# Kernel tuning notes

Measured on AMD Instinct MI355X. Metric: run time of the kernel, lower is better.

## Reference

```python
import jax, jax.numpy as jnp
import numpy as np

B, T, D, V, MEM = 2, 512, 512, 256, 256


def _gru(x, h0, wih, whh, bih, bhh):
    # x: [B,T,D], h0: [B,D]; torch GRU gate order: r, z, n
    def step(h, xt):
        gi = xt @ wih.T + bih            # [B,3D]
        gh = h @ whh.T + bhh             # [B,3D]
        i_r, i_z, i_n = jnp.split(gi, 3, axis=-1)
        h_r, h_z, h_n = jnp.split(gh, 3, axis=-1)
        r = jax.nn.sigmoid(i_r + h_r)
        z = jax.nn.sigmoid(i_z + h_z)
        n = jnp.tanh(i_n + r * h_n)
        h_new = (1.0 - z) * n + z * h
        return h_new, h_new
    hT, ys = jax.lax.scan(step, h0, jnp.swapaxes(x, 0, 1))
    return jnp.swapaxes(ys, 0, 1), hT


def _layernorm(x, g, b, eps=1e-5):
    m = jnp.mean(x, axis=-1, keepdims=True)
    v = jnp.mean((x - m) ** 2, axis=-1, keepdims=True)
    return (x - m) / jnp.sqrt(v + eps) * g + b


def setup_inputs() -> dict:
    key = jax.random.key(0)
    ks = jax.random.split(key, 24)
    s = 1.0 / np.sqrt(D)
    inp = {
        'x': jax.random.randint(ks[0], (B, T), 0, V, dtype=jnp.int32),
        'h_f': jnp.zeros((1, B, D), jnp.float32),
        'h_s': jnp.zeros((1, B, D), jnp.float32),
        'soma_w': jax.random.normal(ks[1], (V, D), jnp.float32),
        'fast_wih': jax.random.normal(ks[2], (3 * D, D)) * s,
        'fast_whh': jax.random.normal(ks[3], (3 * D, D)) * s,
        'fast_bih': jax.random.normal(ks[4], (3 * D,)) * s,
        'fast_bhh': jax.random.normal(ks[5], (3 * D,)) * s,
        'slow_wih': jax.random.normal(ks[6], (3 * D, D)) * s,
        'slow_whh': jax.random.normal(ks[7], (3 * D, D)) * s,
        'slow_bih': jax.random.normal(ks[8], (3 * D,)) * s,
        'slow_bhh': jax.random.normal(ks[9], (3 * D,)) * s,
        'qkv_w': jax.random.normal(ks[10], (3 * D, D)) * s,
        'qkv_b': jax.random.normal(ks[11], (3 * D,)) * s,
        'gate_w': jax.random.normal(ks[12], (D, D)) * s,
        'gate_b': jax.random.normal(ks[13], (D,)) * s,
        'gate_g': jnp.ones((D,), jnp.float32),
        'gate_bb': jnp.zeros((D,), jnp.float32),
        'mem_bank': jax.random.normal(ks[14], (MEM, D)) * 0.1,
        'hip_qw': jax.random.normal(ks[15], (D, D)) * s,
        'hip_qb': jax.random.normal(ks[16], (D,)) * s,
        'axon_w': jax.random.normal(ks[17], (D, 4 * D)) * (0.5 * s),
        'axon_b': jax.random.normal(ks[18], (D,)) * s,
        'norm_g': jnp.ones((D,), jnp.float32),
        'norm_b': jnp.zeros((D,), jnp.float32),
    }
    return inp


def reference(x, h_f, h_s, soma_w, fast_wih, fast_whh, fast_bih, fast_bhh,
              slow_wih, slow_whh, slow_bih, slow_bhh, qkv_w, qkv_b,
              gate_w, gate_b, gate_g, gate_bb, mem_bank, hip_qw, hip_qb,
              axon_w, axon_b, norm_g, norm_b):
    d = soma_w.shape[1]
    s_in = soma_w[x]  # mod[0] == 1.0
    p_f, hf1 = _gru(s_in, h_f[0], fast_wih, fast_whh, fast_bih, fast_bhh)
    p_s, hs1 = _gru(p_f, h_s[0], slow_wih, slow_whh, slow_bih, slow_bhh)
    # LinearIntentMemory: naive cumulative outer-product linear attention
    qkv = p_s @ qkv_w.T + qkv_b
    q, k, v = jnp.split(qkv, 3, axis=-1)
    q = jax.nn.elu(q) + 1.0
    k = jax.nn.elu(k) + 1.0
    kv_cum = jnp.cumsum(jnp.einsum('bti,btj->btij', k, v), axis=1)  # [B,T,D,D]
    num = jnp.einsum('bti,btij->btj', q, kv_cum)
    den = jnp.einsum('bti,bti->bt', q, jnp.cumsum(k, axis=1))[..., None] + 1e-6
    l_mem = num / den
    # intent gate: Linear -> LayerNorm -> Tanh
    intent = jnp.tanh(_layernorm(p_s @ gate_w.T + gate_b, gate_g, gate_bb))
    # hippocampus: softmax attention over memory bank
    qh = p_s @ hip_qw.T + hip_qb
    attn = qh @ mem_bank.T / jnp.sqrt(jnp.float32(d))
    episodes = jax.nn.softmax(attn, axis=-1) @ mem_bank
    combined = jnp.concatenate([p_f, intent, l_mem, episodes], axis=-1)
    thought = _layernorm(jnp.tanh(combined @ axon_w.T + axon_b), norm_g, norm_b)
    sw = soma_w / jnp.maximum(jnp.linalg.norm(soma_w, axis=-1, keepdims=True), 1e-12)
    logits = (thought @ sw.T) * 16.0
    return (logits, thought, hf1[None], hs1[None])
```

## Files before the change

kernel.cpp:

```cpp
#include <hip/hip_runtime.h>
#include <cstddef>

#define F_ELUQK 1
#define F_CAUSAL 2
#define F_DIV 4
#define F_NN 8
#define F_SCALE 16
#define F_ROWSUM 32
#define FLAG_STRIDE 32
#define L_WGS 64
#define UNITS 8

enum : int {
  OFF_QH = 0,
  OFF_COMB = 524288,
  OFF_PS = OFF_COMB + 2097152,
  OFF_QKV = OFF_PS + 524288,
  OFF_SCORES = OFF_QKV + 1572864,
  OFF_DEN = OFF_SCORES + 524288,
  OFF_TMP = OFF_DEN + 1024,
  OFF_ATTN = OFF_TMP + 524288,
  OFF_SWN = OFF_ATTN + 262144,
  OFF_RING = OFF_SWN + 256,
  OFF_HSB = OFF_RING + 8192,
  OFF_FLAGS = OFF_HSB + 4096
};

__global__ __launch_bounds__(256) void gemm(
    const float* __restrict__ A, int lda, const float* __restrict__ B, int ldb,
    float* __restrict__ C, int ldc, int coff, int K,
    const float* __restrict__ bias, const float* __restrict__ den,
    const float* __restrict__ cscale, float* __restrict__ rsum,
    float scale, int flags, int bBatch,
    float* __restrict__ Cz, int kzoff) {
  __shared__ float As[16 * 65];
  __shared__ float Bs[16 * 65];
  int tid = threadIdx.x;
  int n0 = blockIdx.x * 64, m0 = blockIdx.y * 64;
  if (blockIdx.z) { A += kzoff; B += kzoff; C = Cz; bias = nullptr; }
  int rowoff = (m0 >> 9) * bBatch;
  int tx = tid & 15, ty = tid >> 4;

  if ((flags & F_CAUSAL) && n0 > ((m0 & 511) + 63)) {
    #pragma unroll
    for (int i = 0; i < 4; ++i)
      #pragma unroll
      for (int j = 0; j < 4; ++j)
        C[(size_t)(m0 + ty * 4 + i) * ldc + coff + n0 + tx * 4 + j] = 0.f;
    return;
  }

  float acc[4][4] = {};
  for (int k0 = 0; k0 < K; k0 += 16) {
    {
      int rr = tid >> 2, c4 = (tid & 3) << 2;
      const float* ap = A + (size_t)(m0 + rr) * lda + (k0 + c4);
      float4 av = *(const float4*)ap;
      As[(c4 + 0) * 65 + rr] = av.x;
      As[(c4 + 1) * 65 + rr] = av.y;
      As[(c4 + 2) * 65 + rr] = av.z;
      As[(c4 + 3) * 65 + rr] = av.w;
    }
    if (!(flags & F_NN)) {
      int rr = tid >> 2, c4 = (tid & 3) << 2;
      const float* bp = B + (size_t)(n0 + rr + rowoff) * ldb + (k0 + c4);
      float4 bv = *(const float4*)bp;
      Bs[(c4 + 0) * 65 + rr] = bv.x; Bs[(c4 + 1) * 65 + rr] = bv.y;
      Bs[(c4 + 2) * 65 + rr] = bv.z; Bs[(c4 + 3) * 65 + rr] = bv.w;
    } else {
      int kk = tid >> 4, n4 = (tid & 15) << 2;
      const float* bp = B + (size_t)(k0 + kk + rowoff) * ldb + (n0 + n4);
      float4 bv = *(const float4*)bp;
      Bs[kk * 65 + n4 + 0] = bv.x; Bs[kk * 65 + n4 + 1] = bv.y;
      Bs[kk * 65 + n4 + 2] = bv.z; Bs[kk * 65 + n4 + 3] = bv.w;
    }
    __syncthreads();
    #pragma unroll
    for (int k = 0; k < 16; ++k) {
      float av[4], bv[4];
      #pragma unroll
      for (int i = 0; i < 4; ++i) av[i] = As[k * 65 + ty * 4 + i];
      #pragma unroll
      for (int j = 0; j < 4; ++j) bv[j] = Bs[k * 65 + tx * 4 + j];
      #pragma unroll
      for (int i = 0; i < 4; ++i)
        #pragma unroll
        for (int j = 0; j < 4; ++j)
          acc[i][j] = fmaf(av[i], bv[j], acc[i][j]);
    }
    __syncthreads();
  }
  float rs[4] = {0.f, 0.f, 0.f, 0.f};
  #pragma unroll
  for (int i = 0; i < 4; ++i) {
    int m = m0 + ty * 4 + i;
    float dv = (flags & F_DIV) ? (1.0f / (den[m] + 1e-6f)) : 1.0f;
    #pragma unroll
    for (int j = 0; j < 4; ++j) {
      int n = n0 + tx * 4 + j;
      float v = acc[i][j];
      if (bias) v += bias[n];
      if (flags & F_ELUQK) { if (n < 1024) v = (v > 0.f) ? (v + 1.f) : __expf(v); }
      if (flags & F_CAUSAL) { if (n > (m & 511)) v = 0.f; }
      if (flags & F_SCALE) v *= scale;
      if (cscale) v *= cscale[coff + n];
      if (flags & F_DIV) v *= dv;
      C[(size_t)m * ldc + coff + n] = v;
      if (flags & F_ROWSUM) rs[i] += v;
    }
  }
  if (flags & F_ROWSUM) {
    #pragma unroll
    for (int i = 0; i < 4; ++i) {
      float s = rs[i];
      s += __shfl_xor(s, 1); s += __shfl_xor(s, 2);
      s += __shfl_xor(s, 4); s += __shfl_xor(s, 8);
      if (tx == 0) atomicAdd(rsum + (m0 + ty * 4 + i), s);
    }
  }
}

__global__ __launch_bounds__(256) void gemm3(
    const float* __restrict__ A,
    const float* __restrict__ qkvw, const float* __restrict__ qkvb,
    const float* __restrict__ gatew, const float* __restrict__ gateb,
    const float* __restrict__ hipw, const float* __restrict__ hipb,
    float* __restrict__ QKV, float* __restrict__ TMP, float* __restrict__ QH) {
  __shared__ float As[16 * 65];
  __shared__ float Bs[16 * 65];
  int tid = threadIdx.x;
  int n0 = blockIdx.x * 64, m0 = blockIdx.y * 64;
  const float* B; const float* bias; float* C; int ldc, base;
  if (n0 < 1536) { B = qkvw; bias = qkvb; C = QKV; ldc = 1536; base = 0; }
  else if (n0 < 2048) { B = gatew; bias = gateb; C = TMP; ldc = 512; base = 1536; }
  else { B = hipw; bias = hipb; C = QH; ldc = 512; base = 2048; }
  int tx = tid & 15, ty = tid >> 4;
  float acc[4][4] = {};
  for (int k0 = 0; k0 < 512; k0 += 16) {
    {
      int rr = tid >> 2, c4 = (tid & 3) << 2;
      const float* ap = A + (size_t)(m0 + rr) * 512 + (k0 + c4);
      float4 av = *(const float4*)ap;
      As[(c4 + 0) * 65 + rr] = av.x; As[(c4 + 1) * 65 + rr] = av.y;
      As[(c4 + 2) * 65 + rr] = av.z; As[(c4 + 3) * 65 + rr] = av.w;
    }
    {
      int rr = tid >> 2, c4 = (tid & 3) << 2;
      const float* bp = B + (size_t)(n0 - base + rr) * 512 + (k0 + c4);
      float4 bv = *(const float4*)bp;
      Bs[(c4 + 0) * 65 + rr] = bv.x; Bs[(c4 + 1) * 65 + rr] = bv.y;
      Bs[(c4 + 2) * 65 + rr] = bv.z; Bs[(c4 + 3) * 65 + rr] = bv.w;
    }
    __syncthreads();
    #pragma unroll
    for (int k = 0; k < 16; ++k) {
      float av[4], bv[4];
      #pragma unroll
      for (int i = 0; i < 4; ++i) av[i] = As[k * 65 + ty * 4 + i];
      #pragma unroll
      for (int j = 0; j < 4; ++j) bv[j] = Bs[k * 65 + tx * 4 + j];
      #pragma unroll
      for (int i = 0; i < 4; ++i)
        #pragma unroll
        for (int j = 0; j < 4; ++j)
          acc[i][j] = fmaf(av[i], bv[j], acc[i][j]);
    }
    __syncthreads();
  }
  #pragma unroll
  for (int i = 0; i < 4; ++i) {
    int m = m0 + ty * 4 + i;
    #pragma unroll
    for (int j = 0; j < 4; ++j) {
      int n = n0 + tx * 4 + j;
      float v = acc[i][j] + bias[n - base];
      if (n < 1024) v = (v > 0.f) ? (v + 1.f) : __expf(v);
      C[(size_t)m * ldc + (n - base)] = v;
    }
  }
}

__device__ __forceinline__ void post_flag(unsigned* flags, int w, unsigned v) {
  __hip_atomic_store(flags + (size_t)w * FLAG_STRIDE, v, __ATOMIC_RELAXED,
                     __HIP_MEMORY_SCOPE_AGENT);
}
__device__ __forceinline__ void poll64(const unsigned* flags, unsigned tgt, int lane) {
  const unsigned* p = flags + (size_t)lane * FLAG_STRIDE;
  while (__hip_atomic_load(p, __ATOMIC_RELAXED, __HIP_MEMORY_SCOPE_AGENT) < tgt)
    __builtin_amdgcn_s_sleep(1);
}

__global__ __launch_bounds__(256, 1) void gru2_kernel(
    const float* __restrict__ soma, const int* __restrict__ x,
    const float* __restrict__ fwih, const float* __restrict__ fbih,
    const float* __restrict__ fwhh, const float* __restrict__ fbhh,
    const float* __restrict__ h0f,
    const float* __restrict__ swih, const float* __restrict__ sbih,
    const float* __restrict__ swhh, const float* __restrict__ sbhh,
    const float* __restrict__ h0s,
    float* __restrict__ pf_out,
    float* __restrict__ ps_out,
    float* __restrict__ hfT, float* __restrict__ hsT,
    unsigned long long* __restrict__ ringq,
    unsigned long long* __restrict__ hsq,
    unsigned* __restrict__ flagsB) {
  __shared__ __attribute__((aligned(16))) float hl[1024];
  __shared__ __attribute__((aligned(16))) float inb[2048];
  __shared__ float P[48];
  __shared__ float Q[48];
  __shared__ float bl[24];
  __shared__ float bi[24];
  __shared__ int xl[1024];
  int tid = threadIdx.x, wg = blockIdx.x;
  bool L1 = wg < L_WGS;
  int j0 = (wg & (L_WGS - 1)) * UNITS;
  int part = tid & 7, r = tid >> 3;
  int g = r >> 3, u = r & 7;
  int wave = tid >> 6, lane = tid & 63;
  const float* whh = L1 ? fwhh : swhh;
  const float* bhh = L1 ? fbhh : sbhh;
  const float* wih = L1 ? fwih : swih;
  const float* bih = L1 ? fbih : sbih;

  float4 wh[16], wi[16];
  if (r < 24) {
    const float* wp = whh + (size_t)(g * 512 + j0 + u) * 512 + part * 4;
    #pragma unroll
    for (int i = 0; i < 16; ++i) wh[i] = *(const float4*)(wp + i * 32);
    const float* wp2 = wih + (size_t)(g * 512 + j0 + u) * 512 + part * 4;
    #pragma unroll
    for (int i = 0; i < 16; ++i) wi[i] = *(const float4*)(wp2 + i * 32);
  }
  if (tid < 24) {
    bl[tid] = bhh[(tid >> 3) * 512 + j0 + (tid & 7)];
    bi[tid] = bih[(tid >> 3) * 512 + j0 + (tid & 7)];
  }
  if (L1) {
    for (int q = tid; q < 1024; q += 256) xl[q] = x[q];
  }
  __syncthreads();

  const float4* h4 = (const float4*)hl;

  if (L1) {
    for (int t = 0; t < 512; ++t) {
      if (wave == 0) {
        if (t == 0) {
          #pragma unroll
          for (int k = 0; k < 16; ++k) hl[k * 64 + lane] = h0f[k * 64 + lane];
        } else {
          const unsigned long long* s8 = ringq + (size_t)((t - 1) & 3) * 1024;
          unsigned expect = (unsigned)t;
          unsigned long long v[16];
          for (;;) {
            #pragma unroll
            for (int k = 0; k < 16; ++k)
              v[k] = __hip_atomic_load(s8 + k * 64 + lane, __ATOMIC_RELAXED,
                                       __HIP_MEMORY_SCOPE_AGENT);
            unsigned bad = 0;
            #pragma unroll
            for (int k = 0; k < 16; ++k) bad |= ((unsigned)(v[k] >> 32)) ^ expect;
            if (__all(bad == 0)) break;
            __builtin_amdgcn_s_sleep(1);
          }
          #pragma unroll
          for (int k = 0; k < 16; ++k)
            hl[k * 64 + lane] = __uint_as_float((unsigned)v[k]);
        }
      } else if (wave == 1) {
        if (t >= 4) poll64(flagsB, (unsigned)(t - 3), lane);
      } else {
        int b = wave - 2;
        if (t == 0) {
          int row0 = xl[b * 512];
          const float4* sp = (const float4*)(soma + (size_t)row0 * 512);
          float4* dst = (float4*)(inb + b * 512);
          dst[lane * 2] = sp[lane * 2]; dst[lane * 2 + 1] = sp[lane * 2 + 1];
        }
        if (t + 1 < 512) {
          int row = xl[b * 512 + t + 1];
          const float4* sp = (const float4*)(soma + (size_t)row * 512);
          float4* dst = (float4*)(inb + ((t + 1) & 1) * 1024 + b * 512);
          dst[lane * 2] = sp[lane * 2]; dst[lane * 2 + 1] = sp[lane * 2 + 1];
        }
      }
      __syncthreads();
      if (r < 24) {
        const float4* f4v = (const float4*)(inb + (t & 1) * 1024);
        float a0 = 0.f, a1 = 0.f, c0 = 0.f, c1 = 0.f;
        #pragma unroll
        for (int i = 0; i < 16; ++i) {
          float4 w = wh[i];
          float4 x0 = h4[i * 8 + part];
          float4 x1 = h4[128 + i * 8 + part];
          a0 += w.x * x0.x + w.y * x0.y + w.z * x0.z + w.w * x0.w;
          a1 += w.x * x1.x + w.y * x1.y + w.z * x1.z + w.w * x1.w;
          float4 v = wi[i];
          float4 y0 = f4v[i * 8 + part];
          float4 y1 = f4v[128 + i * 8 + part];
          c0 += v.x * y0.x + v.y * y0.y + v.z * y0.z + v.w * y0.w;
          c1 += v.x * y1.x + v.y * y1.y + v.z * y1.z + v.w * y1.w;
        }
        a0 += __shfl_xor(a0, 1); a0 += __shfl_xor(a0, 2); a0 += __shfl_xor(a0, 4);
        a1 += __shfl_xor(a1, 1); a1 += __shfl_xor(a1, 2); a1 += __shfl_xor(a1, 4);
        c0 += __shfl_xor(c0, 1); c0 += __shfl_xor(c0, 2); c0 += __shfl_xor(c0, 4);
        c1 += __shfl_xor(c1, 1); c1 += __shfl_xor(c1, 2); c1 += __shfl_xor(c1, 4);
        if (part == 0) { P[r] = a0; P[24 + r] = a1; Q[r] = c0; Q[24 + r] = c1; }
      }
      __syncthreads();
      if (tid < 16) {
        int b = tid >> 3, u2 = tid & 7, j = j0 + u2;
        float i_r = Q[b * 24 + u2] + bi[u2];
        float i_z = Q[b * 24 + 8 + u2] + bi[8 + u2];
        float i_n = Q[b * 24 + 16 + u2] + bi[16 + u2];
        float gh_r = P[b * 24 + u2] + bl[u2];
        float gh_z = P[b * 24 + 8 + u2] + bl[8 + u2];
        float gh_n = P[b * 24 + 16 + u2] + bl[16 + u2];
        float hold = hl[b * 512 + j];
        float rg = 1.0f / (1.0f + __expf(-(i_r + gh_r)));
        float zg = 1.0f / (1.0f + __expf(-(i_z + gh_z)));
        float ng = tanhf(i_n + rg * gh_n);
        float hnew = (1.0f - zg) * ng + zg * hold;
        unsigned long long pv =
            ((unsigned long long)(unsigned)(t + 1) << 32) |
            (unsigned long long)__float_as_uint(hnew);
        __hip_atomic_store(ringq + (size_t)(t & 3) * 1024 + b * 512 + j, pv,
                           __ATOMIC_RELAXED, __HIP_MEMORY_SCOPE_AGENT);
        pf_out[(size_t)(b * 512 + t) * 2048 + j] = hnew;
        if (t == 511) hfT[b * 512 + j] = hnew;
      }
      __asm__ __volatile__("s_barrier" ::: "memory");
    }
  } else {
    for (int t2 = 0; t2 < 512; ++t2) {
      if (wave == 0) {
        const unsigned long long* f8 = ringq + (size_t)(t2 & 3) * 1024;
        unsigned expect = (unsigned)(t2 + 1);
        unsigned long long v[16];
        for (;;) {
          #pragma unroll
          for (int k = 0; k < 16; ++k)
            v[k] = __hip_atomic_load(f8 + k * 64 + lane, __ATOMIC_RELAXED,
                                     __HIP_MEMORY_SCOPE_AGENT);
          unsigned bad = 0;
          #pragma unroll
          for (int k = 0; k < 16; ++k) bad |= ((unsigned)(v[k] >> 32)) ^ expect;
          if (__all(bad == 0)) break;
          __builtin_amdgcn_s_sleep(1);
        }
        #pragma unroll
        for (int k = 0; k < 16; ++k)
          inb[(t2 & 1) * 1024 + k * 64 + lane] = __uint_as_float((unsigned)v[k]);
        if (lane == 0) post_flag(flagsB, wg - L_WGS, (unsigned)(t2 + 1));
      } else if (wave == 1) {
        if (t2 == 0) {
          #pragma unroll
          for (int k = 0; k < 16; ++k) hl[k * 64 + lane] = h0s[k * 64 + lane];
        } else {
          const unsigned long long* s8 = hsq + (size_t)((t2 - 1) & 1) * 1024;
          unsigned expect = (unsigned)t2;
          unsigned long long v[16];
          for (;;) {
            #pragma unroll
            for (int k = 0; k < 16; ++k)
              v[k] = __hip_atomic_load(s8 + k * 64 + lane, __ATOMIC_RELAXED,
                                       __HIP_MEMORY_SCOPE_AGENT);
            unsigned bad = 0;
            #pragma unroll
            for (int k = 0; k < 16; ++k) bad |= ((unsigned)(v[k] >> 32)) ^ expect;
            if (__all(bad == 0)) break;
            __builtin_amdgcn_s_sleep(1);
          }
          #pragma unroll
          for (int k = 0; k < 16; ++k)
            hl[k * 64 + lane] = __uint_as_float((unsigned)v[k]);
        }
      }
      __syncthreads();
      if (r < 24) {
        const float4* f4v = (const float4*)(inb + (t2 & 1) * 1024);
        float a0 = 0.f, a1 = 0.f, c0 = 0.f, c1 = 0.f;
        #pragma unroll
        for (int i = 0; i < 16; ++i) {
          float4 w = wh[i];
          float4 x0 = h4[i * 8 + part];
          float4 x1 = h4[128 + i * 8 + part];
          a0 += w.x * x0.x + w.y * x0.y + w.z * x0.z + w.w * x0.w;
          a1 += w.x * x1.x + w.y * x1.y + w.z * x1.z + w.w * x1.w;
          float4 v = wi[i];
          float4 y0 = f4v[i * 8 + part];
          float4 y1 = f4v[128 + i * 8 + part];
          c0 += v.x * y0.x + v.y * y0.y + v.z * y0.z + v.w * y0.w;
          c1 += v.x * y1.x + v.y * y1.y + v.z * y1.z + v.w * y1.w;
        }
        a0 += __shfl_xor(a0, 1); a0 += __shfl_xor(a0, 2); a0 += __shfl_xor(a0, 4);
        a1 += __shfl_xor(a1, 1); a1 += __shfl_xor(a1, 2); a1 += __shfl_xor(a1, 4);
        c0 += __shfl_xor(c0, 1); c0 += __shfl_xor(c0, 2); c0 += __shfl_xor(c0, 4);
        c1 += __shfl_xor(c1, 1); c1 += __shfl_xor(c1, 2); c1 += __shfl_xor(c1, 4);
        if (part == 0) { P[r] = a0; P[24 + r] = a1; Q[r] = c0; Q[24 + r] = c1; }
      }
      __syncthreads();
      if (tid < 16) {
        int b = tid >> 3, u2 = tid & 7, j = j0 + u2;
        float i_r = Q[b * 24 + u2] + bi[u2];
        float i_z = Q[b * 24 + 8 + u2] + bi[8 + u2];
        float i_n = Q[b * 24 + 16 + u2] + bi[16 + u2];
        float gh_r = P[b * 24 + u2] + bl[u2];
        float gh_z = P[b * 24 + 8 + u2] + bl[8 + u2];
        float gh_n = P[b * 24 + 16 + u2] + bl[16 + u2];
        float hold = hl[b * 512 + j];
        float rg = 1.0f / (1.0f + __expf(-(i_r + gh_r)));
        float zg = 1.0f / (1.0f + __expf(-(i_z + gh_z)));
        float ng = tanhf(i_n + rg * gh_n);
        float hnew = (1.0f - zg) * ng + zg * hold;
        unsigned long long pv =
            ((unsigned long long)(unsigned)(t2 + 1) << 32) |
            (unsigned long long)__float_as_uint(hnew);
        __hip_atomic_store(hsq + (size_t)(t2 & 1) * 1024 + b * 512 + j, pv,
                           __ATOMIC_RELAXED, __HIP_MEMORY_SCOPE_AGENT);
        ps_out[(size_t)(b * 512 + t2) * 512 + j] = hnew;
        if (t2 == 511) hsT[b * 512 + j] = hnew;
      }
      __asm__ __volatile__("s_barrier" ::: "memory");
    }
  }
}

__global__ __launch_bounds__(256) void softmax_kernel(float* __restrict__ a) {
  int m = blockIdx.x, tid = threadIdx.x;
  float v = a[(size_t)m * 256 + tid];
  float mx = v;
  #pragma unroll
  for (int off = 32; off > 0; off >>= 1) mx = fmaxf(mx, __shfl_down(mx, off));
  __shared__ float r4[4];
  __shared__ float s4[4];
  if ((tid & 63) == 0) r4[tid >> 6] = mx;
  __syncthreads();
  mx = fmaxf(fmaxf(r4[0], r4[1]), fmaxf(r4[2], r4[3]));
  float e = __expf(v - mx);
  float s = e;
  #pragma unroll
  for (int off = 32; off > 0; off >>= 1) s += __shfl_down(s, off);
  if ((tid & 63) == 0) s4[tid >> 6] = s;
  __syncthreads();
  s = s4[0] + s4[1] + s4[2] + s4[3];
  a[(size_t)m * 256 + tid] = e / s;
}

__global__ __launch_bounds__(256) void ln_kernel(
    const float* __restrict__ src, const float* __restrict__ src2,
    float* __restrict__ dst, int ldd, int dcoff,
    const float* __restrict__ gv, const float* __restrict__ bv, int tanhFirst) {
  int m = blockIdx.x, tid = threadIdx.x;
  float x0 = src[(size_t)m * 512 + tid];
  float x1 = src[(size_t)m * 512 + 256 + tid];
  if (src2) { x0 += src2[(size_t)m * 512 + tid]; x1 += src2[(size_t)m * 512 + 256 + tid]; }
  if (tanhFirst) { x0 = tanhf(x0); x1 = tanhf(x1); }
  float s = x0 + x1, ss = x0 * x0 + x1 * x1;
  #pragma unroll
  for (int off = 32; off > 0; off >>= 1) { s += __shfl_down(s, off); ss += __shfl_down(ss, off); }
  __shared__ float rs[4], rss[4];
  if ((tid & 63) == 0) { rs[tid >> 6] = s; rss[tid >> 6] = ss; }
  __syncthreads();
  float st = rs[0] + rs[1] + rs[2] + rs[3];
  float sst = rss[0] + rss[1] + rss[2] + rss[3];
  float mean = st * (1.0f / 512.0f);
  float var = sst * (1.0f / 512.0f) - mean * mean;
  float inv = rsqrtf(var + 1e-5f);
  float y0 = (x0 - mean) * inv * gv[tid] + bv[tid];
  float y1 = (x1 - mean) * inv * gv[256 + tid] + bv[256 + tid];
  if (!tanhFirst) { y0 = tanhf(y0); y1 = tanhf(y1); }
  dst[(size_t)m * ldd + dcoff + tid] = y0;
  dst[(size_t)m * ldd + dcoff + 256 + tid] = y1;
}

__global__ __launch_bounds__(256) void swinv_kernel(const float* __restrict__ soma,
                                                    float* __restrict__ swn) {
  int r = blockIdx.x, tid = threadIdx.x;
  float x0 = soma[(size_t)r * 512 + tid];
  float x1 = soma[(size_t)r * 512 + 256 + tid];
  float ss = x0 * x0 + x1 * x1;
  #pragma unroll
  for (int off = 32; off > 0; off >>= 1) ss += __shfl_down(ss, off);
  __shared__ float r4[4];
  if ((tid & 63) == 0) r4[tid >> 6] = ss;
  __syncthreads();
  if (tid == 0) {
    float norm = fmaxf(sqrtf(r4[0] + r4[1] + r4[2] + r4[3]), 1e-12f);
    swn[r] = 16.0f / norm;
  }
}

extern "C" void kernel_launch(void* const* d_in, const int* in_sizes, int n_in,
                              void* d_out, int out_size, void* d_ws, size_t ws_size,
                              hipStream_t stream) {
  (void)in_sizes; (void)n_in; (void)out_size; (void)ws_size;
  float* W = (float*)d_ws;
  float* outf = (float*)d_out;
  const int* x = (const int*)d_in[0];
  const float* soma = (const float*)d_in[3];

  hipMemsetAsync((char*)d_ws + (size_t)OFF_RING * 4, 0, 57344, stream);
  hipMemsetAsync((char*)d_ws + (size_t)OFF_DEN * 4, 0, 4096, stream);

  gru2_kernel<<<2 * L_WGS, 256, 0, stream>>>(soma, x,
      (const float*)d_in[4], (const float*)d_in[6],
      (const float*)d_in[5], (const float*)d_in[7], (const float*)d_in[1],
      (const float*)d_in[8], (const float*)d_in[10],
      (const float*)d_in[9], (const float*)d_in[11], (const float*)d_in[2],
      W + OFF_COMB, W + OFF_PS, outf + 786432, outf + 787456,
      (unsigned long long*)(W + OFF_RING), (unsigned long long*)(W + OFF_HSB),
      (unsigned*)(W + OFF_FLAGS));

  gemm3<<<dim3(40, 16), 256, 0, stream>>>(W + OFF_PS,
      (const float*)d_in[12], (const float*)d_in[13],
      (const float*)d_in[14], (const float*)d_in[15],
      (const float*)d_in[19], (const float*)d_in[20],
      W + OFF_QKV, W + OFF_TMP, W + OFF_QH);

  gemm<<<dim3(8, 16), 256, 0, stream>>>(W + OFF_QKV, 1536, W + OFF_QKV + 512, 1536,
      W + OFF_SCORES, 512, 0, 512, nullptr, nullptr, nullptr, W + OFF_DEN,
      1.f, F_CAUSAL | F_ROWSUM, 512, nullptr, 0);

  gemm<<<dim3(8, 16), 256, 0, stream>>>(W + OFF_SCORES, 512, W + OFF_QKV + 1024, 1536,
      W + OFF_COMB, 2048, 1024, 512, nullptr, W + OFF_DEN, nullptr, nullptr,
      1.f, F_NN | F_DIV, 512, nullptr, 0);

  ln_kernel<<<1024, 256, 0, stream>>>(W + OFF_TMP, nullptr, W + OFF_COMB, 2048, 512,
      (const float*)d_in[16], (const float*)d_in[17], 0);

  gemm<<<dim3(4, 16), 256, 0, stream>>>(W + OFF_QH, 512, (const float*)d_in[18], 512,
      W + OFF_ATTN, 256, 0, 512, nullptr, nullptr, nullptr, nullptr,
      0.04419417382415922f, F_SCALE, 0, nullptr, 0);
  softmax_kernel<<<1024, 256, 0, stream>>>(W + OFF_ATTN);
  gemm<<<dim3(8, 16), 256, 0, stream>>>(W + OFF_ATTN, 256, (const float*)d_in[18], 512,
      W + OFF_COMB, 2048, 1536, 256, nullptr, nullptr, nullptr, nullptr,
      1.f, F_NN, 0, nullptr, 0);

  gemm<<<dim3(8, 16, 2), 256, 0, stream>>>(W + OFF_COMB, 2048, (const float*)d_in[21], 2048,
      W + OFF_TMP, 512, 0, 1024, (const float*)d_in[22], nullptr, nullptr, nullptr,
      1.f, 0, 0, W + OFF_QH, 1024);

  ln_kernel<<<1024, 256, 0, stream>>>(W + OFF_TMP, W + OFF_QH, outf + 262144, 512, 0,
      (const float*)d_in[23], (const float*)d_in[24], 1);

  swinv_kernel<<<256, 256, 0, stream>>>(soma, W + OFF_SWN);
  gemm<<<dim3(4, 16), 256, 0, stream>>>(outf + 262144, 512, soma, 512,
      outf, 256, 0, 512, nullptr, nullptr, W + OFF_SWN, nullptr,
      1.f, 0, 0, nullptr, 0);
}
```

Before: 2.104 ms.

## Restructure GRU step pipeline: precompute input projection before barrier, add per-WG flags

Reorganizes the persistent two-layer GRU kernel so waves 0-2 compute the input-side projection (wih·x) before the first barrier while wave 3 polls for the previous hidden state. The input fetch for the next step, including the slow layer's read of the fast ring, moves into the slot after the barrier, overlapping with the recurrent matvec. Per-workgroup flags (flagsA) are added so the ring is polled on cheap flag words before the tagged 64-bit loads. Barriers become lgkmcnt-wait plus s_barrier. This aims to take the input projection and prefetch off the serial critical path, at the cost of an extra flag store per step and a larger zeroed region.

Result: faster. 1.790 ms (-14.9%).

```diff
diff --git a/kernel.cpp b/kernel.cpp
--- a/kernel.cpp
+++ b/kernel.cpp
@@ -25,6 +25,8 @@
   OFF_HSB = OFF_RING + 8192,
   OFF_FLAGS = OFF_HSB + 4096
 };
+
+#define BAR() __asm__ __volatile__("s_waitcnt lgkmcnt(0)\n\ts_barrier" ::: "memory")
 
 __global__ __launch_bounds__(256) void gemm(
     const float* __restrict__ A, int lda, const float* __restrict__ B, int ldb,
@@ -189,6 +191,25 @@
   while (__hip_atomic_load(p, __ATOMIC_RELAXED, __HIP_MEMORY_SCOPE_AGENT) < tgt)
     __builtin_amdgcn_s_sleep(1);
 }
+__device__ __forceinline__ void tagload16(const unsigned long long* __restrict__ src,
+                                          unsigned expect, int lane,
+                                          float* __restrict__ dstLds) {
+  unsigned long long v[16];
+  for (;;) {
+    #pragma unroll
+    for (int k = 0; k < 16; ++k)
+      v[k] = __hip_atomic_load(src + k * 64 + lane, __ATOMIC_RELAXED,
+                               __HIP_MEMORY_SCOPE_AGENT);
+    unsigned bad = 0;
+    #pragma unroll
+    for (int k = 0; k < 16; ++k) bad |= ((unsigned)(v[k] >> 32)) ^ expect;
+    if (__all(bad == 0)) break;
+    __builtin_amdgcn_s_sleep(1);
+  }
+  #pragma unroll
+  for (int k = 0; k < 16; ++k)
+    dstLds[k * 64 + lane] = __uint_as_float((unsigned)v[k]);
+}
 
 __global__ __launch_bounds__(256, 1) void gru2_kernel(
     const float* __restrict__ soma, const int* __restrict__ x,
@@ -203,7 +224,7 @@
     float* __restrict__ hfT, float* __restrict__ hsT,
     unsigned long long* __restrict__ ringq,
     unsigned long long* __restrict__ hsq,
-    unsigned* __restrict__ flagsB) {
+    unsigned* __restrict__ flagsA, unsigned* __restrict__ flagsB) {
   __shared__ __attribute__((aligned(16))) float hl[1024];
   __shared__ __attribute__((aligned(16))) float inb[2048];
   __shared__ float P[48];
@@ -240,54 +261,48 @@
   }
   __syncthreads();
 
+  if (wave == 3) {
+    if (L1) {
+      int r0 = xl[0], r1 = xl[512];
+      const float4* sp0 = (const float4*)(soma + (size_t)r0 * 512);
+      const float4* sp1 = (const float4*)(soma + (size_t)r1 * 512);
+      float4* dst = (float4*)inb;
+      dst[lane * 2] = sp0[lane * 2]; dst[lane * 2 + 1] = sp0[lane * 2 + 1];
+      dst[128 + lane * 2] = sp1[lane * 2]; dst[128 + lane * 2 + 1] = sp1[lane * 2 + 1];
+    } else {
+      poll64(flagsA, 1u, lane);
+      tagload16(ringq, 1u, lane, inb);
+    }
+  }
+  BAR();
+
   const float4* h4 = (const float4*)hl;
 
   if (L1) {
     for (int t = 0; t < 512; ++t) {
-      if (wave == 0) {
+      float c0 = 0.f, c1 = 0.f;
+      if (wave == 3) {
         if (t == 0) {
           #pragma unroll
           for (int k = 0; k < 16; ++k) hl[k * 64 + lane] = h0f[k * 64 + lane];
         } else {
-          const unsigned long long* s8 = ringq + (size_t)((t - 1) & 3) * 1024;
-          unsigned expect = (unsigned)t;
-          unsigned long long v[16];
-          for (;;) {
-            #pragma unroll
-            for (int k = 0; k < 16; ++k)
-              v[k] = __hip_atomic_load(s8 + k * 64 + lane, __ATOMIC_RELAXED,
-                                       __HIP_MEMORY_SCOPE_AGENT);
-            unsigned bad = 0;
-            #pragma unroll
-            for (int k = 0; k < 16; ++k) bad |= ((unsigned)(v[k] >> 32)) ^ expect;
-            if (__all(bad == 0)) break;
-            __builtin_amdgcn_s_sleep(1);
-          }
-          #pragma unroll
-          for (int k = 0; k < 16; ++k)
-            hl[k * 64 + lane] = __uint_as_float((unsigned)v[k]);
-        }
-      } else if (wave == 1) {
-        if (t >= 4) poll64(flagsB, (unsigned)(t - 3), lane);
+          poll64(flagsA, (unsigned)t, lane);
+          tagload16(ringq + (size_t)((t - 1) & 3) * 1024, (unsigned)t, lane, hl);
+        }
       } else {
-        int b = wave - 2;
-        if (t == 0) {
-          int row0 = xl[b * 512];
-          const float4* sp = (const float4*)(soma + (size_t)row0 * 512);
-          float4* dst = (float4*)(inb + b * 512);
-          dst[lane * 2] = sp[lane * 2]; dst[lane * 2 + 1] = sp[lane * 2 + 1];
-        }
-        if (t + 1 < 512) {
-          int row = xl[b * 512 + t + 1];
-          const float4* sp = (const float4*)(soma + (size_t)row * 512);
-          float4* dst = (float4*)(inb + ((t + 1) & 1) * 1024 + b * 512);
-          dst[lane * 2] = sp[lane * 2]; dst[lane * 2 + 1] = sp[lane * 2 + 1];
+        const float4* f4v = (const float4*)(inb + (t & 1) * 1024);
+        #pragma unroll
+        for (int i = 0; i < 16; ++i) {
+          float4 v = wi[i];
+          float4 y0 = f4v[i * 8 + part];
+          float4 y1 = f4v[128 + i * 8 + part];
+          c0 += v.x * y0.x + v.y * y0.y + v.z * y0.z + v.w * y0.w;
+          c1 += v.x * y1.x + v.y * y1.y + v.z * y1.z + v.w * y1.w;
         }
       }
-      __syncthreads();
-      if (r < 24) {
-        const float4* f4v = (const float4*)(inb + (t & 1) * 1024);
-        float a0 = 0.f, a1 = 0.f, c0 = 0.f, c1 = 0.f;
+      BAR();
+      if (wave != 3) {
+        float a0 = 0.f, a1 = 0.f;
         #pragma unroll
         for (int i = 0; i < 16; ++i) {
           float4 w = wh[i];
@@ -295,21 +310,30 @@
           float4 x1 = h4[128 + i * 8 + part];
           a0 += w.x * x0.x + w.y * x0.y + w.z * x0.z + w.w * x0.w;
           a1 += w.x * x1.x + w.y * x1.y + w.z * x1.z + w.w * x1.w;
-          float4 v = wi[i];
-          float4 y0 = f4v[i * 8 + part];
-          float4 y1 = f4v[128 + i * 8 + part];
-          c0 += v.x * y0.x + v.y * y0.y + v.z * y0.z + v.w * y0.w;
-          c1 += v.x * y1.x + v.y * y1.y + v.z * y1.z + v.w * y1.w;
         }
         a0 += __shfl_xor(a0, 1); a0 += __shfl_xor(a0, 2); a0 += __shfl_xor(a0, 4);
         a1 += __shfl_xor(a1, 1); a1 += __shfl_xor(a1, 2); a1 += __shfl_xor(a1, 4);
         c0 += __shfl_xor(c0, 1); c0 += __shfl_xor(c0, 2); c0 += __shfl_xor(c0, 4);
         c1 += __shfl_xor(c1, 1); c1 += __shfl_xor(c1, 2); c1 += __shfl_xor(c1, 4);
         if (part == 0) { P[r] = a0; P[24 + r] = a1; Q[r] = c0; Q[24 + r] = c1; }
+      } else {
+        if (t + 1 < 512) {
+          int r0 = xl[t + 1], r1 = xl[512 + t + 1];
+          const float4* sp0 = (const float4*)(soma + (size_t)r0 * 512);
+          const float4* sp1 = (const float4*)(soma + (size_t)r1 * 512);
+          float4 p0 = sp0[lane * 2], p1 = sp0[lane * 2 + 1];
+          float4 p2 = sp1[lane * 2], p3 = sp1[lane * 2 + 1];
+          if (t >= 4) poll64(flagsB, (unsigned)(t - 3), lane);
+          float4* dst = (float4*)(inb + ((t + 1) & 1) * 1024);
+          dst[lane * 2] = p0; dst[lane * 2 + 1] = p1;
+          dst[128 + lane * 2] = p2; dst[128 + lane * 2 + 1] = p3;
+        } else {
+          if (t >= 4) poll64(flagsB, (unsigned)(t - 3), lane);
+        }
       }
-      __syncthreads();
-      if (tid < 16) {
-        int b = tid >> 3, u2 = tid & 7, j = j0 + u2;
+      BAR();
+      if (wave == 3 && lane < 16) {
+        int b = lane >> 3, u2 = lane & 7, j = j0 + u2;
         float i_r = Q[b * 24 + u2] + bi[u2];
         float i_z = Q[b * 24 + 8 + u2] + bi[8 + u2];
         float i_n = Q[b * 24 + 16 + u2] + bi[16 + u2];
@@ -326,60 +350,36 @@
             (unsigned long long)__float_as_uint(hnew);
         __hip_atomic_store(ringq + (size_t)(t & 3) * 1024 + b * 512 + j, pv,
                            __ATOMIC_RELAXED, __HIP_MEMORY_SCOPE_AGENT);
+        if (lane == 0) post_flag(flagsA, wg, (unsigned)(t + 1));
         pf_out[(size_t)(b * 512 + t) * 2048 + j] = hnew;
         if (t == 511) hfT[b * 512 + j] = hnew;
       }
-      __asm__ __volatile__("s_barrier" ::: "memory");
     }
   } else {
     for (int t2 = 0; t2 < 512; ++t2) {
-      if (wave == 0) {
-        const unsigned long long* f8 = ringq + (size_t)(t2 & 3) * 1024;
-        unsigned expect = (unsigned)(t2 + 1);
-        unsigned long long v[16];
-        for (;;) {
-          #pragma unroll
-          for (int k = 0; k < 16; ++k)
-            v[k] = __hip_atomic_load(f8 + k * 64 + lane, __ATOMIC_RELAXED,
-                                     __HIP_MEMORY_SCOPE_AGENT);
-          unsigned bad = 0;
-          #pragma unroll
-          for (int k = 0; k < 16; ++k) bad |= ((unsigned)(v[k] >> 32)) ^ expect;
-          if (__all(bad == 0)) break;
-          __builtin_amdgcn_s_sleep(1);
-        }
-        #pragma unroll
-        for (int k = 0; k < 16; ++k)
-          inb[(t2 & 1) * 1024 + k * 64 + lane] = __uint_as_float((unsigned)v[k]);
-        if (lane == 0) post_flag(flagsB, wg - L_WGS, (unsigned)(t2 + 1));
-      } else if (wave == 1) {
+      float c0 = 0.f, c1 = 0.f;
+      if (wave == 3) {
         if (t2 == 0) {
           #pragma unroll
           for (int k = 0; k < 16; ++k) hl[k * 64 + lane] = h0s[k * 64 + lane];
         } else {
-          const unsigned long long* s8 = hsq + (size_t)((t2 - 1) & 1) * 1024;
-          unsigned expect = (unsigned)t2;
-          unsigned long long v[16];
-          for (;;) {
-            #pragma unroll
-            for (int k = 0; k < 16; ++k)
-              v[k] = __hip_atomic_load(s8 + k * 64 + lane, __ATOMIC_RELAXED,
-                                       __HIP_MEMORY_SCOPE_AGENT);
-            unsigned bad = 0;
-            #pragma unroll
-            for (int k = 0; k < 16; ++k) bad |= ((unsigned)(v[k] >> 32)) ^ expect;
-            if (__all(bad == 0)) break;
-            __builtin_amdgcn_s_sleep(1);
-          }
-          #pragma unroll
-          for (int k = 0; k < 16; ++k)
-            hl[k * 64 + lane] = __uint_as_float((unsigned)v[k]);
+          poll64(flagsB, (unsigned)t2, lane);
+          tagload16(hsq + (size_t)((t2 - 1) & 1) * 1024, (unsigned)t2, lane, hl);
+        }
+      } else {
+        const float4* f4v = (const float4*)(inb + (t2 & 1) * 1024);
+        #pragma unroll
+        for (int i = 0; i < 16; ++i) {
+          float4 v = wi[i];
+          float4 y0 = f4v[i * 8 + part];
+          float4 y1 = f4v[128 + i * 8 + part];
+          c0 += v.x * y0.x + v.y * y0.y + v.z * y0.z + v.w * y0.w;
+          c1 += v.x * y1.x + v.y * y1.y + v.z * y1.z + v.w * y1.w;
         }
       }
-      __syncthreads();
-      if (r < 24) {
-        const float4* f4v = (const float4*)(inb + (t2 & 1) * 1024);
-        float a0 = 0.f, a1 = 0.f, c0 = 0.f, c1 = 0.f;
+      BAR();
+      if (wave != 3) {
+        float a0 = 0.f, a1 = 0.f;
         #pragma unroll
         for (int i = 0; i < 16; ++i) {
           float4 w = wh[i];
@@ -387,21 +387,22 @@
           float4 x1 = h4[128 + i * 8 + part];
           a0 += w.x * x0.x + w.y * x0.y + w.z * x0.z + w.w * x0.w;
           a1 += w.x * x1.x + w.y * x1.y + w.z * x1.z + w.w * x1.w;
-          float4 v = wi[i];
-          float4 y0 = f4v[i * 8 + part];
-          float4 y1 = f4v[128 + i * 8 + part];
-          c0 += v.x * y0.x + v.y * y0.y + v.z * y0.z + v.w * y0.w;
-          c1 += v.x * y1.x + v.y * y1.y + v.z * y1.z + v.w * y1.w;
         }
         a0 += __shfl_xor(a0, 1); a0 += __shfl_xor(a0, 2); a0 += __shfl_xor(a0, 4);
         a1 += __shfl_xor(a1, 1); a1 += __shfl_xor(a1, 2); a1 += __shfl_xor(a1, 4);
         c0 += __shfl_xor(c0, 1); c0 += __shfl_xor(c0, 2); c0 += __shfl_xor(c0, 4);
         c1 += __shfl_xor(c1, 1); c1 += __shfl_xor(c1, 2); c1 += __shfl_xor(c1, 4);
         if (part == 0) { P[r] = a0; P[24 + r] = a1; Q[r] = c0; Q[24 + r] = c1; }
+      } else {
+        if (t2 + 1 < 512) {
+          poll64(flagsA, (unsigned)(t2 + 2), lane);
+          tagload16(ringq + (size_t)((t2 + 1) & 3) * 1024, (unsigned)(t2 + 2),
+                    lane, inb + ((t2 + 1) & 1) * 1024);
+        }
       }
-      __syncthreads();
-      if (tid < 16) {
-        int b = tid >> 3, u2 = tid & 7, j = j0 + u2;
+      BAR();
+      if (wave == 3 && lane < 16) {
+        int b = lane >> 3, u2 = lane & 7, j = j0 + u2;
         float i_r = Q[b * 24 + u2] + bi[u2];
         float i_z = Q[b * 24 + 8 + u2] + bi[8 + u2];
         float i_n = Q[b * 24 + 16 + u2] + bi[16 + u2];
@@ -418,10 +419,10 @@
             (unsigned long long)__float_as_uint(hnew);
         __hip_atomic_store(hsq + (size_t)(t2 & 1) * 1024 + b * 512 + j, pv,
                            __ATOMIC_RELAXED, __HIP_MEMORY_SCOPE_AGENT);
+        if (lane == 0) post_flag(flagsB, wg - L_WGS, (unsigned)(t2 + 1));
         ps_out[(size_t)(b * 512 + t2) * 512 + j] = hnew;
         if (t2 == 511) hsT[b * 512 + j] = hnew;
       }
-      __asm__ __volatile__("s_barrier" ::: "memory");
     }
   }
 }
@@ -500,7 +501,7 @@
   const int* x = (const int*)d_in[0];
   const float* soma = (const float*)d_in[3];
 
-  hipMemsetAsync((char*)d_ws + (size_t)OFF_RING * 4, 0, 57344, stream);
+  hipMemsetAsync((char*)d_ws + (size_t)OFF_RING * 4, 0, 65536, stream);
   hipMemsetAsync((char*)d_ws + (size_t)OFF_DEN * 4, 0, 4096, stream);
 
   gru2_kernel<<<2 * L_WGS, 256, 0, stream>>>(soma, x,
@@ -510,7 +511,8 @@
       (const float*)d_in[9], (const float*)d_in[11], (const float*)d_in[2],
       W + OFF_COMB, W + OFF_PS, outf + 786432, outf + 787456,
       (unsigned long long*)(W + OFF_RING), (unsigned long long*)(W + OFF_HSB),
-      (unsigned*)(W + OFF_FLAGS));
+      (unsigned*)(W + OFF_FLAGS),
+      (unsigned*)(W + OFF_FLAGS) + L_WGS * FLAG_STRIDE);
 
   gemm3<<<dim3(40, 16), 256, 0, stream>>>(W + OFF_PS,
       (const float*)d_in[12], (const float*)d_in[13],
```
